# Optimization experiments

Hardware: AMD Instinct MI355X
Metric: run time of the kernel (lower is better)

Reference implementation:

```python
import jax, jax.numpy as jnp
import numpy as np

MARGIN = 0.3


def _pairwise_dist(x):
    # Exact euclidean cdist; same math as torch.cdist's non-mm mode:
    # sqrt(sum_k (x_i[k]-x_j[k])^2) == sqrt(|x_i|^2 + |x_j|^2 - 2 x_i.x_j).
    sq = jnp.sum(x * x, axis=1)
    sqd = sq[:, None] + sq[None, :] - 2.0 * (x @ x.T)
    sqd = jnp.maximum(sqd, 0.0)
    # safe sqrt: zero distance (diagonal) -> dist 0 with zero grad, like torch
    safe = jnp.where(sqd > 0, sqd, 1.0)
    return jnp.where(sqd > 0, jnp.sqrt(safe), 0.0)


def setup_inputs() -> dict:
    key = jax.random.key(0)
    k1, k2 = jax.random.split(key)
    n, d, n_classes = 8192, 128, 64
    inputs = jax.random.normal(k1, (n, d), dtype=jnp.float32)
    targets = jax.random.randint(k2, (n,), 0, n_classes)
    return {"inputs": inputs, "targets": targets}


def reference(inputs, targets):
    dist = _pairwise_dist(inputs)  # (n, n)
    mask = targets[:, None] == targets[None, :]  # (n, n) same-label mask
    # hard positive: max distance among same-label (diag included, as in torch code)
    dist_ap = jnp.max(jnp.where(mask, dist, -jnp.inf), axis=1)  # (n,)
    # hard negative: min distance among different-label
    dist_an = jnp.min(jnp.where(mask, jnp.inf, dist), axis=1)  # (n,)
    # MarginRankingLoss with y=1: mean(relu(-(dist_an - dist_ap) + margin))
    loss = jnp.mean(jax.nn.relu(dist_ap - dist_an + MARGIN))
    return (loss, dist)
```

## Files before the change

kernel.cpp:

```cpp
#include <hip/hip_runtime.h>
#include <hip/hip_bf16.h>
#include <cstdint>
#include <cstddef>


#define NROWS 8192
#define DIMK  128
#define MARGIN 0.3f

typedef __bf16 bf16x8 __attribute__((ext_vector_type(8)));
typedef float  f32x4  __attribute__((ext_vector_type(4)));
typedef float  f32x2  __attribute__((ext_vector_type(2)));
typedef int    i32x4  __attribute__((ext_vector_type(4)));

__device__ __forceinline__ unsigned short f2bf(float f) {
    unsigned u = __float_as_uint(f);
    u += 0x7fffu + ((u >> 16) & 1u);
    return (unsigned short)(u >> 16);
}

__global__ __launch_bounds__(256) void prep_kernel(
    const float* __restrict__ X, unsigned short* __restrict__ Xb,
    float* __restrict__ sq, int* __restrict__ ap, int* __restrict__ an)
{
    const int t = blockIdx.x * 256 + threadIdx.x;
    if (t < NROWS) { ap[t] = 0; an[t] = 0x7f800000; }
    const int row  = t >> 6;
    const int lane = t & 63;
    const f32x2 v = *(const f32x2*)(X + (size_t)row * DIMK + lane * 2);
    const unsigned short b0 = f2bf(v[0]);
    const unsigned short b1 = f2bf(v[1]);
    const int swz = (row & 7) << 4;
    *(unsigned*)((char*)Xb + (size_t)row * 256 + ((lane * 4) ^ swz)) =
        (unsigned)b0 | ((unsigned)b1 << 16);
    const float f0 = __uint_as_float((unsigned)b0 << 16);
    const float f1 = __uint_as_float((unsigned)b1 << 16);
    float s = f0 * f0 + f1 * f1;
    #pragma unroll
    for (int off = 32; off; off >>= 1) s += __shfl_xor(s, off);
    if (lane == 0) sq[row] = s;
}

__global__ __launch_bounds__(256, 2) void dist_kernel(
    const unsigned short* __restrict__ Xb, const float* __restrict__ sq,
    const int* __restrict__ tgt, float* __restrict__ dist,
    int* __restrict__ ap, int* __restrict__ an)
{
    __shared__ __align__(16) char lds[64 * 1024];

    const int t  = threadIdx.x;
    const int bm = blockIdx.x, bn = blockIdx.y;

    {
        const char* gA = (const char*)Xb + (size_t)bm * 32768;
        const char* gB = (const char*)Xb + (size_t)bn * 32768;
        #pragma unroll
        for (int i = 0; i < 8; i++) {
            const int off = i * 4096 + t * 16;
            __builtin_amdgcn_global_load_lds(
                (const __attribute__((address_space(1))) void*)(gA + off),
                (__attribute__((address_space(3))) void*)(lds + off),
                16, 0, 0);
            __builtin_amdgcn_global_load_lds(
                (const __attribute__((address_space(1))) void*)(gB + off),
                (__attribute__((address_space(3))) void*)(lds + 32768 + off),
                16, 0, 0);
        }
    }
    __syncthreads();

    const int lane = t & 63, wave = t >> 6;
    const int wm = (wave >> 1) * 64, wn = (wave & 1) * 64;
    const int l15 = lane & 15, quad = lane >> 4;

    f32x4 acc[4][4];
    #pragma unroll
    for (int mi = 0; mi < 4; mi++)
        #pragma unroll
        for (int ni = 0; ni < 4; ni++)
            acc[mi][ni] = (f32x4){0.f, 0.f, 0.f, 0.f};

    #pragma unroll
    for (int ks = 0; ks < 4; ks++) {
        const int kb2 = ks * 64 + quad * 16;
        bf16x8 a_frag[4], b_frag[4];
        #pragma unroll
        for (int mi = 0; mi < 4; mi++) {
            const int r = wm + mi * 16 + l15;
            a_frag[mi] = *(const bf16x8*)(lds + r * 256 + (kb2 ^ ((r & 7) << 4)));
        }
        #pragma unroll
        for (int ni = 0; ni < 4; ni++) {
            const int c = wn + ni * 16 + l15;
            b_frag[ni] = *(const bf16x8*)(lds + 32768 + c * 256 + (kb2 ^ ((c & 7) << 4)));
        }
        #pragma unroll
        for (int mi = 0; mi < 4; mi++)
            #pragma unroll
            for (int ni = 0; ni < 4; ni++)
                acc[mi][ni] = __builtin_amdgcn_mfma_f32_16x16x32_bf16(
                    a_frag[mi], b_frag[ni], acc[mi][ni], 0, 0, 0);
    }

    __syncthreads();

    const int rbase = bm * 128;
    const int cbase = bn * 128;
    const float INF = __int_as_float(0x7f800000);

    float sqc[4]; int lc[4];
    #pragma unroll
    for (int ni = 0; ni < 4; ni++) {
        lc[ni]  = wn + ni * 16 + l15;
        sqc[ni] = sq[cbase + lc[ni]];
    }

    #pragma unroll
    for (int mi = 0; mi < 4; mi++) {
        const int rl0 = wm + mi * 16 + quad * 4;
        const f32x4 sqr = *(const f32x4*)(sq + rbase + rl0);
        #pragma unroll
        for (int reg = 0; reg < 4; reg++) {
            const int rl  = rl0 + reg;
            const int rg  = rbase + rl;
            const int swz = (rl & 7) << 4;
            #pragma unroll
            for (int ni = 0; ni < 4; ni++) {
                const float dot = acc[mi][ni][reg];
                float sqd = sqr[reg] + sqc[ni] - 2.0f * dot;
                float d = sqd > 0.0f ? sqrtf(sqd) : 0.0f;
                if (rg == cbase + lc[ni]) d = 0.0f;
                *(float*)(lds + rl * 512 + ((lc[ni] << 2) ^ swz)) = d;
            }
        }
    }
    __syncthreads();

    #pragma unroll 4
    for (int it = 0; it < 16; it++) {
        const int idx = it * 256 + t;
        const int r   = idx >> 5;
        const int rc  = idx & 31;
        const f32x4 d4 = *(const f32x4*)(lds + r * 512 + ((rc ^ (r & 7)) << 4));
        const int rg = rbase + r;
        float* drow = dist + (size_t)rg * NROWS + cbase;

        const float prev = __shfl_up(d4[3], 1);
        if (rc == 0) {
            __builtin_nontemporal_store(d4[0], drow);
            const f32x2 v01 = {d4[1], d4[2]};
            __builtin_nontemporal_store(v01, (f32x2*)(drow + 1));
        } else {
            const f32x4 v = {prev, d4[0], d4[1], d4[2]};
            __builtin_nontemporal_store(v, (f32x4*)(drow + (rc << 2) - 1));
        }
        if (rc == 31)
            __builtin_nontemporal_store(d4[3], drow + 127);

        const int  trg = tgt[rg];
        const i32x4 tc = *(const i32x4*)(tgt + cbase + (rc << 2));
        float apv = -1.0f, anv = INF;
        #pragma unroll
        for (int j = 0; j < 4; j++) {
            const bool same = (trg == tc[j]);
            apv = fmaxf(apv, same ? d4[j] : -1.0f);
            anv = fminf(anv, same ? INF : d4[j]);
        }
        #pragma unroll
        for (int m = 1; m < 32; m <<= 1) {
            apv = fmaxf(apv, __shfl_xor(apv, m));
            anv = fminf(anv, __shfl_xor(anv, m));
        }
        if ((t & 31) == 0) {
            atomicMax(ap + rg, __float_as_int(apv));
            atomicMin(an + rg, __float_as_int(anv));
        }
    }
}

__global__ __launch_bounds__(256) void loss_kernel(
    const int* __restrict__ ap, const int* __restrict__ an,
    float* __restrict__ out)
{
    __shared__ float red[4];
    float s = 0.0f;
    for (int i = threadIdx.x; i < NROWS; i += 256) {
        const float v = __int_as_float(ap[i]) - __int_as_float(an[i]) + MARGIN;
        s += v > 0.0f ? v : 0.0f;
    }
    #pragma unroll
    for (int off = 32; off; off >>= 1) s += __shfl_xor(s, off);
    if ((threadIdx.x & 63) == 0) red[threadIdx.x >> 6] = s;
    __syncthreads();
    if (threadIdx.x == 0)
        out[0] = (red[0] + red[1] + red[2] + red[3]) * (1.0f / NROWS);
}

extern "C" void kernel_launch(void* const* d_in, const int* in_sizes, int n_in,
                              void* d_out, int out_size, void* d_ws, size_t ws_size,
                              hipStream_t stream)
{
    const float* X   = (const float*)d_in[0];
    const int*   tgt = (const int*)d_in[1];
    float*       out = (float*)d_out;

    unsigned short* Xb = (unsigned short*)d_ws;
    float* sq = (float*)((char*)d_ws + (size_t)NROWS * DIMK * 2);
    int*   ap = (int*)(sq + NROWS);
    int*   an = ap + NROWS;

    prep_kernel<<<(NROWS * 64) / 256, 256, 0, stream>>>(X, Xb, sq, ap, an);

    dim3 grid(64, 64);
    dist_kernel<<<grid, 256, 0, stream>>>(Xb, sq, tgt, out + 1, ap, an);

    loss_kernel<<<1, 256, 0, stream>>>(ap, an, out);
}
```

Measured before the change: 396.2 us.

## Exploit distance symmetry: compute upper-triangle tiles and write both halves

The distance kernel launches only the upper-triangular 128x128 tile pairs (2080 blocks). Each block writes its tile and, for off-diagonal tiles, the transposed tile as well, updating the hard positive/negative reductions for both row and column indices with per-column atomics. Operand fragments now load straight from global memory instead of being staged through LDS, the epilogue staging buffer is halved to 32KB, and occupancy is raised to 3 blocks per SIMD. This halves the MFMA work and the operand loads, at the cost of a transposed write path, extra synchronisation and more atomics per block.

```diff
diff --git a/kernel.cpp b/kernel.cpp
--- a/kernel.cpp
+++ b/kernel.cpp
@@ -30,8 +30,7 @@
     const f32x2 v = *(const f32x2*)(X + (size_t)row * DIMK + lane * 2);
     const unsigned short b0 = f2bf(v[0]);
     const unsigned short b1 = f2bf(v[1]);
-    const int swz = (row & 7) << 4;
-    *(unsigned*)((char*)Xb + (size_t)row * 256 + ((lane * 4) ^ swz)) =
+    *(unsigned*)(Xb + (size_t)row * DIMK + lane * 2) =
         (unsigned)b0 | ((unsigned)b1 << 16);
     const float f0 = __uint_as_float((unsigned)b0 << 16);
     const float f1 = __uint_as_float((unsigned)b1 << 16);
@@ -41,37 +40,40 @@
     if (lane == 0) sq[row] = s;
 }
 
-__global__ __launch_bounds__(256, 2) void dist_kernel(
+__device__ __forceinline__ void store_row_shifted(float* drow, f32x4 d4, int rc) {
+    const float prev = __shfl_up(d4[3], 1);
+    if (rc == 0) {
+        __builtin_nontemporal_store(d4[0], drow);
+        const f32x2 v01 = {d4[1], d4[2]};
+        __builtin_nontemporal_store(v01, (f32x2*)(drow + 1));
+    } else {
+        const f32x4 v = {prev, d4[0], d4[1], d4[2]};
+        __builtin_nontemporal_store(v, (f32x4*)(drow + (rc << 2) - 1));
+    }
+    if (rc == 31)
+        __builtin_nontemporal_store(d4[3], drow + 127);
+}
+
+__global__ __launch_bounds__(256, 3) void dist_kernel(
     const unsigned short* __restrict__ Xb, const float* __restrict__ sq,
     const int* __restrict__ tgt, float* __restrict__ dist,
     int* __restrict__ ap, int* __restrict__ an)
 {
-    __shared__ __align__(16) char lds[64 * 1024];
-
-    const int t  = threadIdx.x;
-    const int bm = blockIdx.x, bn = blockIdx.y;
-
-    {
-        const char* gA = (const char*)Xb + (size_t)bm * 32768;
-        const char* gB = (const char*)Xb + (size_t)bn * 32768;
-        #pragma unroll
-        for (int i = 0; i < 8; i++) {
-            const int off = i * 4096 + t * 16;
-            __builtin_amdgcn_global_load_lds(
-                (const __attribute__((address_space(1))) void*)(gA + off),
-                (__attribute__((address_space(3))) void*)(lds + off),
-                16, 0, 0);
-            __builtin_amdgcn_global_load_lds(
-                (const __attribute__((address_space(1))) void*)(gB + off),
-                (__attribute__((address_space(3))) void*)(lds + 32768 + off),
-                16, 0, 0);
-        }
-    }
-    __syncthreads();
-
+    __shared__ __align__(16) char lds[32 * 1024];
+
+    const int bid = blockIdx.x;
+    int bm = (int)(0.5f * (129.0f - sqrtf(129.0f * 129.0f - 8.0f * (float)bid)));
+    while ((bm + 1) * (129 - (bm + 1)) / 2 <= bid) bm++;
+    while (bm * (129 - bm) / 2 > bid) bm--;
+    const int bn = bm + (bid - bm * (129 - bm) / 2);
+
+    const int t = threadIdx.x;
     const int lane = t & 63, wave = t >> 6;
-    const int wm = (wave >> 1) * 64, wn = (wave & 1) * 64;
+    const int wm = (wave >> 1) << 6;
+    const int wn = (wave & 1) << 6;
     const int l15 = lane & 15, quad = lane >> 4;
+    const int rbase = bm << 7, cbase = bn << 7;
+    const float INF = __int_as_float(0x7f800000);
 
     f32x4 acc[4][4];
     #pragma unroll
@@ -80,100 +82,152 @@
         for (int ni = 0; ni < 4; ni++)
             acc[mi][ni] = (f32x4){0.f, 0.f, 0.f, 0.f};
 
+    const unsigned short* Arow = Xb + (size_t)(rbase + wm + l15) * DIMK;
+    const unsigned short* Brow = Xb + (size_t)(cbase + wn + l15) * DIMK;
     #pragma unroll
     for (int ks = 0; ks < 4; ks++) {
-        const int kb2 = ks * 64 + quad * 16;
-        bf16x8 a_frag[4], b_frag[4];
-        #pragma unroll
-        for (int mi = 0; mi < 4; mi++) {
-            const int r = wm + mi * 16 + l15;
-            a_frag[mi] = *(const bf16x8*)(lds + r * 256 + (kb2 ^ ((r & 7) << 4)));
-        }
-        #pragma unroll
-        for (int ni = 0; ni < 4; ni++) {
-            const int c = wn + ni * 16 + l15;
-            b_frag[ni] = *(const bf16x8*)(lds + 32768 + c * 256 + (kb2 ^ ((c & 7) << 4)));
-        }
+        const int kb = ks * 32 + quad * 8;
+        bf16x8 af[4], bfr[4];
+        #pragma unroll
+        for (int mi = 0; mi < 4; mi++)
+            af[mi] = *(const bf16x8*)(Arow + mi * 16 * DIMK + kb);
+        #pragma unroll
+        for (int ni = 0; ni < 4; ni++)
+            bfr[ni] = *(const bf16x8*)(Brow + ni * 16 * DIMK + kb);
         #pragma unroll
         for (int mi = 0; mi < 4; mi++)
             #pragma unroll
             for (int ni = 0; ni < 4; ni++)
                 acc[mi][ni] = __builtin_amdgcn_mfma_f32_16x16x32_bf16(
-                    a_frag[mi], b_frag[ni], acc[mi][ni], 0, 0, 0);
-    }
-
-    __syncthreads();
-
-    const int rbase = bm * 128;
-    const int cbase = bn * 128;
-    const float INF = __int_as_float(0x7f800000);
-
-    float sqc[4]; int lc[4];
+                    af[mi], bfr[ni], acc[mi][ni], 0, 0, 0);
+    }
+
+    int lcv[4]; float sqc[4];
     #pragma unroll
     for (int ni = 0; ni < 4; ni++) {
-        lc[ni]  = wn + ni * 16 + l15;
-        sqc[ni] = sq[cbase + lc[ni]];
-    }
-
+        lcv[ni] = wn + ni * 16 + l15;
+        sqc[ni] = sq[cbase + lcv[ni]];
+    }
+    const bool diag = (bm == bn);
     #pragma unroll
     for (int mi = 0; mi < 4; mi++) {
         const int rl0 = wm + mi * 16 + quad * 4;
         const f32x4 sqr = *(const f32x4*)(sq + rbase + rl0);
         #pragma unroll
         for (int reg = 0; reg < 4; reg++) {
-            const int rl  = rl0 + reg;
-            const int rg  = rbase + rl;
-            const int swz = (rl & 7) << 4;
+            const int rl = rl0 + reg;
             #pragma unroll
             for (int ni = 0; ni < 4; ni++) {
-                const float dot = acc[mi][ni][reg];
-                float sqd = sqr[reg] + sqc[ni] - 2.0f * dot;
+                const float sqd = sqr[reg] + sqc[ni] - 2.0f * acc[mi][ni][reg];
                 float d = sqd > 0.0f ? sqrtf(sqd) : 0.0f;
-                if (rg == cbase + lc[ni]) d = 0.0f;
-                *(float*)(lds + rl * 512 + ((lc[ni] << 2) ^ swz)) = d;
-            }
-        }
-    }
-    __syncthreads();
-
-    #pragma unroll 4
-    for (int it = 0; it < 16; it++) {
-        const int idx = it * 256 + t;
-        const int r   = idx >> 5;
-        const int rc  = idx & 31;
-        const f32x4 d4 = *(const f32x4*)(lds + r * 512 + ((rc ^ (r & 7)) << 4));
-        const int rg = rbase + r;
-        float* drow = dist + (size_t)rg * NROWS + cbase;
-
-        const float prev = __shfl_up(d4[3], 1);
-        if (rc == 0) {
-            __builtin_nontemporal_store(d4[0], drow);
-            const f32x2 v01 = {d4[1], d4[2]};
-            __builtin_nontemporal_store(v01, (f32x2*)(drow + 1));
-        } else {
-            const f32x4 v = {prev, d4[0], d4[1], d4[2]};
-            __builtin_nontemporal_store(v, (f32x4*)(drow + (rc << 2) - 1));
-        }
-        if (rc == 31)
-            __builtin_nontemporal_store(d4[3], drow + 127);
-
-        const int  trg = tgt[rg];
-        const i32x4 tc = *(const i32x4*)(tgt + cbase + (rc << 2));
-        float apv = -1.0f, anv = INF;
+                if (diag && rl == lcv[ni]) d = 0.0f;
+                acc[mi][ni][reg] = d;
+            }
+        }
+    }
+
+    const int rc   = t & 31;
+    const int rsel = t >> 5;
+
+    {
+        float apv[4] = {-1.f, -1.f, -1.f, -1.f};
+        float anv[4] = {INF, INF, INF, INF};
+        const i32x4 tc = *(const i32x4*)(tgt + cbase + rc * 4);
+        #pragma unroll
+        for (int h = 0; h < 2; h++) {
+            __syncthreads();
+            if (wm == h * 64) {
+                #pragma unroll
+                for (int mi = 0; mi < 4; mi++) {
+                    #pragma unroll
+                    for (int reg = 0; reg < 4; reg++) {
+                        const int r = mi * 16 + quad * 4 + reg;
+                        const int sw = ((r >> 2) & 1) << 6;
+                        #pragma unroll
+                        for (int ni = 0; ni < 4; ni++)
+                            *(float*)(lds + r * 512 + ((lcv[ni] << 2) ^ sw)) =
+                                acc[mi][ni][reg];
+                    }
+                }
+            }
+            __syncthreads();
+            #pragma unroll
+            for (int it = 0; it < 8; it++) {
+                const int r = it * 8 + rsel;
+                const f32x4 d4 = *(const f32x4*)(
+                    lds + r * 512 + ((rc << 4) ^ ((((r >> 2) & 1)) << 6)));
+                const int rowg = rbase + h * 64 + r;
+                store_row_shifted(dist + (size_t)rowg * NROWS + cbase, d4, rc);
+                const int trg = tgt[rowg];
+                #pragma unroll
+                for (int j = 0; j < 4; j++) {
+                    const bool same = (trg == tc[j]);
+                    apv[j] = fmaxf(apv[j], same ? d4[j] : -1.f);
+                    anv[j] = fminf(anv[j], same ? INF : d4[j]);
+                }
+            }
+        }
         #pragma unroll
         for (int j = 0; j < 4; j++) {
-            const bool same = (trg == tc[j]);
-            apv = fmaxf(apv, same ? d4[j] : -1.0f);
-            anv = fminf(anv, same ? INF : d4[j]);
-        }
-        #pragma unroll
-        for (int m = 1; m < 32; m <<= 1) {
-            apv = fmaxf(apv, __shfl_xor(apv, m));
-            anv = fminf(anv, __shfl_xor(anv, m));
-        }
-        if ((t & 31) == 0) {
-            atomicMax(ap + rg, __float_as_int(apv));
-            atomicMin(an + rg, __float_as_int(anv));
+            apv[j] = fmaxf(apv[j], __shfl_xor(apv[j], 32));
+            anv[j] = fminf(anv[j], __shfl_xor(anv[j], 32));
+        }
+        if (lane < 32) {
+            #pragma unroll
+            for (int j = 0; j < 4; j++) {
+                atomicMax(ap + cbase + rc * 4 + j, __float_as_int(apv[j]));
+                atomicMin(an + cbase + rc * 4 + j, __float_as_int(anv[j]));
+            }
+        }
+    }
+
+    if (!diag) {
+        float apv[4] = {-1.f, -1.f, -1.f, -1.f};
+        float anv[4] = {INF, INF, INF, INF};
+        const i32x4 tc = *(const i32x4*)(tgt + rbase + rc * 4);
+        #pragma unroll
+        for (int h = 0; h < 2; h++) {
+            __syncthreads();
+            if (wn == h * 64) {
+                #pragma unroll
+                for (int ni = 0; ni < 4; ni++) {
+                    const int cl = ni * 16 + l15;
+                    #pragma unroll
+                    for (int mi = 0; mi < 4; mi++) {
+                        const int rl0 = wm + mi * 16 + quad * 4;
+                        *(f32x4*)(lds + cl * 512 +
+                                  ((rl0 << 2) ^ ((cl & 7) << 4))) = acc[mi][ni];
+                    }
+                }
+            }
+            __syncthreads();
+            #pragma unroll
+            for (int it = 0; it < 8; it++) {
+                const int c = it * 8 + rsel;
+                const f32x4 d4 = *(const f32x4*)(
+                    lds + c * 512 + ((rc << 4) ^ ((c & 7) << 4)));
+                const int rowg = cbase + h * 64 + c;
+                store_row_shifted(dist + (size_t)rowg * NROWS + rbase, d4, rc);
+                const int trg = tgt[rowg];
+                #pragma unroll
+                for (int j = 0; j < 4; j++) {
+                    const bool same = (trg == tc[j]);
+                    apv[j] = fmaxf(apv[j], same ? d4[j] : -1.f);
+                    anv[j] = fminf(anv[j], same ? INF : d4[j]);
+                }
+            }
+        }
+        #pragma unroll
+        for (int j = 0; j < 4; j++) {
+            apv[j] = fmaxf(apv[j], __shfl_xor(apv[j], 32));
+            anv[j] = fminf(anv[j], __shfl_xor(anv[j], 32));
+        }
+        if (lane < 32) {
+            #pragma unroll
+            for (int j = 0; j < 4; j++) {
+                atomicMax(ap + rbase + rc * 4 + j, __float_as_int(apv[j]));
+                atomicMin(an + rbase + rc * 4 + j, __float_as_int(anv[j]));
+            }
         }
     }
 }
@@ -211,8 +265,7 @@
 
     prep_kernel<<<(NROWS * 64) / 256, 256, 0, stream>>>(X, Xb, sq, ap, an);
 
-    dim3 grid(64, 64);
-    dist_kernel<<<grid, 256, 0, stream>>>(Xb, sq, tgt, out + 1, ap, an);
+    dist_kernel<<<2080, 256, 0, stream>>>(Xb, sq, tgt, out + 1, ap, an);
 
     loss_kernel<<<1, 256, 0, stream>>>(ap, an, out);
 }
```

Result: slower. 405.7 us (+2.4%).

## Reduce hard pos/neg per column via symmetry with LDS atomics, drop nontemporal stores

Applied to the files above, without the earlier changes.

Because the distance matrix and label mask are both symmetric, each block now reduces hard-positive and hard-negative values per column, which equals the row-wise result. Each thread keeps running max/min values in registers across all rows it handles. This replaces the per-row 32-lane shuffle reductions and per-row global atomics with one cross-half shuffle, LDS atomics and 128 global atomics per block. The distance stores also switch from nontemporal to ordinary stores, which may change cache behaviour on the large output write.

```diff
diff --git a/kernel.cpp b/kernel.cpp
--- a/kernel.cpp
+++ b/kernel.cpp
@@ -41,15 +41,30 @@
     if (lane == 0) sq[row] = s;
 }
 
+__device__ __forceinline__ void store_row_shifted(float* drow, f32x4 d4, int rc) {
+    const float prev = __shfl_up(d4[3], 1);
+    if (rc == 0) {
+        drow[0] = d4[0];
+        *(f32x2*)(drow + 1) = (f32x2){d4[1], d4[2]};
+    } else {
+        *(f32x4*)(drow + (rc << 2) - 1) = (f32x4){prev, d4[0], d4[1], d4[2]};
+    }
+    if (rc == 31)
+        drow[127] = d4[3];
+}
+
 __global__ __launch_bounds__(256, 2) void dist_kernel(
     const unsigned short* __restrict__ Xb, const float* __restrict__ sq,
     const int* __restrict__ tgt, float* __restrict__ dist,
     int* __restrict__ ap, int* __restrict__ an)
 {
     __shared__ __align__(16) char lds[64 * 1024];
+    __shared__ int apL[128], anL[128];
 
     const int t  = threadIdx.x;
     const int bm = blockIdx.x, bn = blockIdx.y;
+
+    if (t < 128) { apL[t] = 0; anL[t] = 0x7f800000; }
 
     {
         const char* gA = (const char*)Xb + (size_t)bm * 32768;
@@ -70,8 +85,11 @@
     __syncthreads();
 
     const int lane = t & 63, wave = t >> 6;
-    const int wm = (wave >> 1) * 64, wn = (wave & 1) * 64;
+    const int wm = (wave >> 1) << 6;
+    const int wn = (wave & 1) << 6;
     const int l15 = lane & 15, quad = lane >> 4;
+    const int rbase = bm << 7, cbase = bn << 7;
+    const float INF = __int_as_float(0x7f800000);
 
     f32x4 acc[4][4];
     #pragma unroll
@@ -83,38 +101,33 @@
     #pragma unroll
     for (int ks = 0; ks < 4; ks++) {
         const int kb2 = ks * 64 + quad * 16;
-        bf16x8 a_frag[4], b_frag[4];
+        bf16x8 af[4], bfr[4];
         #pragma unroll
         for (int mi = 0; mi < 4; mi++) {
             const int r = wm + mi * 16 + l15;
-            a_frag[mi] = *(const bf16x8*)(lds + r * 256 + (kb2 ^ ((r & 7) << 4)));
+            af[mi] = *(const bf16x8*)(lds + r * 256 + (kb2 ^ ((r & 7) << 4)));
         }
         #pragma unroll
         for (int ni = 0; ni < 4; ni++) {
             const int c = wn + ni * 16 + l15;
-            b_frag[ni] = *(const bf16x8*)(lds + 32768 + c * 256 + (kb2 ^ ((c & 7) << 4)));
+            bfr[ni] = *(const bf16x8*)(lds + 32768 + c * 256 + (kb2 ^ ((c & 7) << 4)));
         }
         #pragma unroll
         for (int mi = 0; mi < 4; mi++)
             #pragma unroll
             for (int ni = 0; ni < 4; ni++)
                 acc[mi][ni] = __builtin_amdgcn_mfma_f32_16x16x32_bf16(
-                    a_frag[mi], b_frag[ni], acc[mi][ni], 0, 0, 0);
-    }
-
-    __syncthreads();
-
-    const int rbase = bm * 128;
-    const int cbase = bn * 128;
-    const float INF = __int_as_float(0x7f800000);
-
-    float sqc[4]; int lc[4];
+                    af[mi], bfr[ni], acc[mi][ni], 0, 0, 0);
+    }
+
+    __syncthreads();
+
+    int lcv[4]; float sqc[4];
     #pragma unroll
     for (int ni = 0; ni < 4; ni++) {
-        lc[ni]  = wn + ni * 16 + l15;
-        sqc[ni] = sq[cbase + lc[ni]];
-    }
-
+        lcv[ni] = wn + ni * 16 + l15;
+        sqc[ni] = sq[cbase + lcv[ni]];
+    }
     #pragma unroll
     for (int mi = 0; mi < 4; mi++) {
         const int rl0 = wm + mi * 16 + quad * 4;
@@ -126,55 +139,51 @@
             const int swz = (rl & 7) << 4;
             #pragma unroll
             for (int ni = 0; ni < 4; ni++) {
-                const float dot = acc[mi][ni][reg];
-                float sqd = sqr[reg] + sqc[ni] - 2.0f * dot;
+                const float sqd = sqr[reg] + sqc[ni] - 2.0f * acc[mi][ni][reg];
                 float d = sqd > 0.0f ? sqrtf(sqd) : 0.0f;
-                if (rg == cbase + lc[ni]) d = 0.0f;
-                *(float*)(lds + rl * 512 + ((lc[ni] << 2) ^ swz)) = d;
+                if (rg == cbase + lcv[ni]) d = 0.0f;
+                *(float*)(lds + rl * 512 + ((lcv[ni] << 2) ^ swz)) = d;
             }
         }
     }
     __syncthreads();
+
+    const int rc = t & 31;
+    const int w  = t >> 5;
+    float apv[4] = {-1.f, -1.f, -1.f, -1.f};
+    float anv[4] = {INF, INF, INF, INF};
+    const i32x4 tc = *(const i32x4*)(tgt + cbase + rc * 4);
 
     #pragma unroll 4
     for (int it = 0; it < 16; it++) {
-        const int idx = it * 256 + t;
-        const int r   = idx >> 5;
-        const int rc  = idx & 31;
+        const int r = it * 8 + w;
         const f32x4 d4 = *(const f32x4*)(lds + r * 512 + ((rc ^ (r & 7)) << 4));
         const int rg = rbase + r;
-        float* drow = dist + (size_t)rg * NROWS + cbase;
-
-        const float prev = __shfl_up(d4[3], 1);
-        if (rc == 0) {
-            __builtin_nontemporal_store(d4[0], drow);
-            const f32x2 v01 = {d4[1], d4[2]};
-            __builtin_nontemporal_store(v01, (f32x2*)(drow + 1));
-        } else {
-            const f32x4 v = {prev, d4[0], d4[1], d4[2]};
-            __builtin_nontemporal_store(v, (f32x4*)(drow + (rc << 2) - 1));
-        }
-        if (rc == 31)
-            __builtin_nontemporal_store(d4[3], drow + 127);
-
-        const int  trg = tgt[rg];
-        const i32x4 tc = *(const i32x4*)(tgt + cbase + (rc << 2));
-        float apv = -1.0f, anv = INF;
+        store_row_shifted(dist + (size_t)rg * NROWS + cbase, d4, rc);
+        const int trg = tgt[rg];
         #pragma unroll
         for (int j = 0; j < 4; j++) {
             const bool same = (trg == tc[j]);
-            apv = fmaxf(apv, same ? d4[j] : -1.0f);
-            anv = fminf(anv, same ? INF : d4[j]);
-        }
-        #pragma unroll
-        for (int m = 1; m < 32; m <<= 1) {
-            apv = fmaxf(apv, __shfl_xor(apv, m));
-            anv = fminf(anv, __shfl_xor(anv, m));
-        }
-        if ((t & 31) == 0) {
-            atomicMax(ap + rg, __float_as_int(apv));
-            atomicMin(an + rg, __float_as_int(anv));
-        }
+            apv[j] = fmaxf(apv[j], same ? d4[j] : -1.f);
+            anv[j] = fminf(anv[j], same ? INF : d4[j]);
+        }
+    }
+    #pragma unroll
+    for (int j = 0; j < 4; j++) {
+        apv[j] = fmaxf(apv[j], __shfl_xor(apv[j], 32));
+        anv[j] = fminf(anv[j], __shfl_xor(anv[j], 32));
+    }
+    if (lane < 32) {
+        #pragma unroll
+        for (int j = 0; j < 4; j++) {
+            atomicMax(apL + rc * 4 + j, __float_as_int(apv[j]));
+            atomicMin(anL + rc * 4 + j, __float_as_int(anv[j]));
+        }
+    }
+    __syncthreads();
+    if (t < 128) {
+        atomicMax(ap + cbase + t, apL[t]);
+        atomicMin(an + cbase + t, anL[t]);
     }
 }
 
```

Measured after the change: 332.5 us. 16.1% less time.
